# Performance work log

Hardware: AMD Instinct MI355X
Metric: run time of the kernel (lower is better)

Reference implementation:

```python
import jax, jax.numpy as jnp
import numpy as np

START_IDX = 1  # PAD_IDX = 0, END_IDX = 2 (unused in teacher-forcing path)
B, N, F = 16, 49, 1024
H, E, V = 1024, 1024, 15000
S, W = 5, 12


def setup_inputs() -> dict:
    key = jax.random.key(0)
    ks = jax.random.split(key, 16)
    def w(k, shape, s=0.02):
        return jax.random.normal(k, shape, dtype=jnp.float32) * s
    emb = w(ks[0], (V, E)).at[0].set(0.0)  # padding_idx = 0
    return dict(
        features=jax.random.normal(ks[1], (B, N, F), dtype=jnp.float32),
        reports=jax.random.randint(ks[2], (B, S, W), 0, V),
        attn_w1=w(ks[3], (F + H, H)), attn_b1=jnp.zeros((H,), jnp.float32),
        attn_w2=w(ks[4], (H, 1)), attn_b2=jnp.zeros((1,), jnp.float32),
        s_wih=w(ks[5], (4 * H, F)), s_whh=w(ks[6], (4 * H, H)),
        s_bih=jnp.zeros((4 * H,), jnp.float32), s_bhh=jnp.zeros((4 * H,), jnp.float32),
        stop_w=w(ks[7], (H, 1)), stop_b=jnp.zeros((1,), jnp.float32),
        emb=emb,
        w_wih=w(ks[8], (4 * H, E)), w_whh=w(ks[9], (4 * H, H)),
        w_bih=jnp.zeros((4 * H,), jnp.float32), w_bhh=jnp.zeros((4 * H,), jnp.float32),
        fc_w=w(ks[10], (H, V)), fc_b=jnp.zeros((V,), jnp.float32),
    )


def _lstm_cell(x, h, c, wih, whh, bih, bhh):
    # PyTorch LSTMCell: gates ordered i, f, g, o
    gates = x @ wih.T + h @ whh.T + (bih + bhh)
    i, f, g, o = jnp.split(gates, 4, axis=-1)
    c = jax.nn.sigmoid(f) * c + jax.nn.sigmoid(i) * jnp.tanh(g)
    h = jax.nn.sigmoid(o) * jnp.tanh(c)
    return h, c


def _attention(features, h, w1, b1, w2, b2):
    # features [B,N,F], h [B,H] -> additive 2-layer attention over N locations
    b, n, _ = features.shape
    hcat = jnp.broadcast_to(h[:, None, :], (b, n, h.shape[-1]))
    x = jnp.concatenate([features, hcat], axis=-1)           # [B,N,F+H]
    e = (jnp.tanh(x @ w1 + b1) @ w2 + b2)[..., 0]            # [B,N]
    scores = jax.nn.softmax(e, axis=-1)
    att = jnp.einsum('bn,bnf->bf', scores, features)          # [B,F]
    return att, scores


def _forward(features, reports, attn_w1, attn_b1, attn_w2, attn_b2,
             s_wih, s_whh, s_bih, s_bhh, stop_w, stop_b, emb,
             w_wih, w_whh, w_bih, w_bhh, fc_w, fc_b):
    bsz = features.shape[0]
    h0 = jnp.zeros((bsz, s_whh.shape[-1]), features.dtype)
    att0, _ = _attention(features, h0, attn_w1, attn_b1, attn_w2, attn_b2)
    start_emb = jnp.broadcast_to(emb[START_IDX][None, :], (bsz, emb.shape[-1]))

    def sentence_step(carry, reports_i):   # reports_i: [W, B] teacher-forcing tokens
        h, c, att = carry
        h, c = _lstm_cell(att, h, c, s_wih, s_whh, s_bih, s_bhh)
        czero = jnp.zeros_like(h)

        def word_step(wc, idx):
            hw, cw, inp = wc
            hw, cw = _lstm_cell(inp, hw, cw, w_wih, w_whh, w_bih, w_bhh)
            pred = hw @ fc_w + fc_b                           # [B,V]
            return (hw, cw, emb[idx]), pred

        # word LSTM initialized with h=topic, c=0; first input = <start> embedding
        _, preds = jax.lax.scan(word_step, (h, czero, start_emb), reports_i)  # [W,B,V]
        stop = jax.nn.sigmoid(h @ stop_w + stop_b)[:, 0]      # [B]
        att, scores = _attention(features, h, attn_w1, attn_b1, attn_w2, attn_b2)
        return (h, c, att), (preds, stop, scores)

    reports_sw = jnp.transpose(reports, (1, 2, 0))            # [S,W,B]
    _, (seq, stops, scores) = jax.lax.scan(sentence_step, (h0, h0, att0), reports_sw)
    seq_out = jnp.transpose(seq, (2, 0, 1, 3))                # [B,S,W,V]
    stops_out = jnp.transpose(stops, (1, 0))                  # [B,S]
    scores_out = jnp.transpose(scores, (1, 0, 2))             # [B,S,N]
    return seq_out, stops_out, scores_out


def reference(features, reports, attn_w1, attn_b1, attn_w2, attn_b2,
              s_wih, s_whh, s_bih, s_bhh, stop_w, stop_b, emb,
              w_wih, w_whh, w_bih, w_bhh, fc_w, fc_b):
    return _forward(features, reports, attn_w1, attn_b1, attn_w2, attn_b2,
                    s_wih, s_whh, s_bih, s_bhh, stop_w, stop_b, emb,
                    w_wih, w_whh, w_bih, w_bhh, fc_w, fc_b)
```

## Files before the change

kernel.cpp:

```cpp
#include <hip/hip_runtime.h>
#include <hip/hip_bf16.h>

#define B_  16
#define S_  5
#define W_  12
#define NL_ 49
#define H_  1024
#define V_  15000
#define SEQ_N   14400000
#define STOP_N  80
#define OUT_STOP (SEQ_N)
#define OUT_SCORE (SEQ_N + STOP_N)

typedef __attribute__((ext_vector_type(8))) short     short8;
typedef __attribute__((ext_vector_type(4))) float     f32x4;
typedef __attribute__((ext_vector_type(4))) unsigned int u32x4;
typedef __attribute__((ext_vector_type(4))) unsigned short us4;

#define OFF_FCWT   0ull
#define OFF_WWHHP  30720000ull
#define OFF_WWIHP  39108608ull
#define OFF_WSCATP 47497216ull
#define OFF_W1AT   64274432ull
#define OFF_W1BT   66371584ull
#define OFF_FBF    68468736ull
#define OFF_XIN    70074368ull
#define OFF_PF     72040448ull
#define OFF_XW     75251712ull
#define OFF_HBALL  90980352ull
#define OFF_HWBF0  92946432ull
#define OFF_HWBF1  93110272ull
#define OFF_ACAT1  93274112ull
#define OFF_H      93339648ull
#define OFF_EVAL   93405184ull
#define OFF_ACAT0  93408384ull
#define OFF_C      93473920ull
#define OFF_CW     93539456ull
#define OFF_HPROJ  93867136ull
#define WS_TOTAL   93932672ull
#define ZERO_BASE  OFF_ACAT0
#define ZERO_BYTES (524288ull)

__device__ __forceinline__ unsigned short f2bf(float x){
  unsigned u = __float_as_uint(x);
  u += 0x7fffu + ((u >> 16) & 1u);
  return (unsigned short)(u >> 16);
}
__device__ __forceinline__ float sigm(float x){ return 1.f/(1.f+expf(-x)); }

typedef __attribute__((address_space(3))) unsigned int  as3_u32;
typedef __attribute__((address_space(1))) const unsigned int as1_u32;

__device__ __forceinline__ void gl16(const void* g, void* l){
  __builtin_amdgcn_global_load_lds((as1_u32*)g, (as3_u32*)l, 16, 0, 0);
}

template<int ROWS,int CH,int NW>
__device__ __forceinline__ void stage_swz(const unsigned short* __restrict__ gbase, int grs,
                                          unsigned short* lds, int wid, int lane,
                                          int r0, int rmax){
  constexpr int RPI = 64/CH;
  constexpr int NISS = ROWS/RPI;
  const int r_in = lane / CH;
  const int cbp  = lane % CH;
  #pragma unroll
  for (int it = wid; it < NISS; it += NW){
    int rl = it*RPI + r_in;
    int gr = r0 + rl; gr = gr < rmax ? gr : rmax-1;
    int cb = cbp ^ (rl & 7);
    gl16(gbase + (size_t)gr*grs + cb*8, lds + it*RPI*CH*8);
  }
}

__device__ __forceinline__ void transp64(const float* __restrict__ src, int sld,
                                         int rb, int cb, int Cc,
                                         unsigned short* __restrict__ dst, int dld,
                                         float (*t)[65])
{
  const int tx = threadIdx.x & 15, ty = threadIdx.x >> 4;
  #pragma unroll
  for (int ii = 0; ii < 4; ii++){
    int r = ty + ii*16;
    int c = cb + tx*4;
    const float* s = src + (size_t)(rb + r)*sld + c;
    f32x4 v;
    if (c + 4 <= Cc) v = *(const f32x4*)s;
    else {
      v[0] = (c   < Cc) ? s[0] : 0.f;
      v[1] = (c+1 < Cc) ? s[1] : 0.f;
      v[2] = (c+2 < Cc) ? s[2] : 0.f;
      v[3] = (c+3 < Cc) ? s[3] : 0.f;
    }
    t[r][tx*4+0]=v[0]; t[r][tx*4+1]=v[1]; t[r][tx*4+2]=v[2]; t[r][tx*4+3]=v[3];
  }
  __syncthreads();
  #pragma unroll
  for (int ii = 0; ii < 4; ii++){
    int c = ty + ii*16;
    if (cb + c < Cc){
      int r4 = tx*4;
      us4 o; o[0]=f2bf(t[r4][c]); o[1]=f2bf(t[r4+1][c]); o[2]=f2bf(t[r4+2][c]); o[3]=f2bf(t[r4+3][c]);
      *(us4*)(dst + (size_t)(cb + c)*dld + rb + r4) = o;
    }
  }
}

#define U0 200704u
#define U1 (U0+1048576u)
#define U2 (U1+1048576u)
#define U3 (U2+1048576u)
#define U4 (U3+1048576u)
#define U5 (U4+245760u)
#define NCVT_BLK 1280
#define NTR_BLK  1068
#define NZ_BLK   16
#define NPREP    (NCVT_BLK + NTR_BLK + NZ_BLK)

__device__ __forceinline__ void cvt_gate_unit(const float* __restrict__ src,
                                              unsigned short* __restrict__ dst,
                                              unsigned e, int dld, int doff){
  int n = e >> 8, cc = (e & 255)*4;
  int gate = (n >> 4) & 3, j = ((n >> 6) << 4) | (n & 15);
  f32x4 v = *(const f32x4*)(src + ((size_t)(gate*1024 + j) << 10) + cc);
  us4 o; o[0]=f2bf(v[0]); o[1]=f2bf(v[1]); o[2]=f2bf(v[2]); o[3]=f2bf(v[3]);
  *(us4*)(dst + (size_t)n*dld + doff + cc) = o;
}

__global__ void k_prep(const float* __restrict__ features,
                       const float* __restrict__ w_whh, const float* __restrict__ w_wih,
                       const float* __restrict__ s_wih, const float* __restrict__ s_whh,
                       const float* __restrict__ emb, const int* __restrict__ reports,
                       const float* __restrict__ attn_w1, const float* __restrict__ fc_w,
                       unsigned short* __restrict__ FBF, unsigned short* __restrict__ WWHHP,
                       unsigned short* __restrict__ WWIHP, unsigned short* __restrict__ WSCATP,
                       unsigned short* __restrict__ XIN,
                       unsigned short* __restrict__ W1AT, unsigned short* __restrict__ W1BT,
                       unsigned short* __restrict__ FCWT, char* __restrict__ zbase)
{
  __shared__ float t[64][65];
  int bx = blockIdx.x;
  if (bx < NCVT_BLK){
    for (unsigned u = bx*256u + threadIdx.x; u < U5; u += NCVT_BLK*256u){
      if (u < U0){
        int idx = u*4;
        f32x4 v = *(const f32x4*)(features + idx);
        us4 o; o[0]=f2bf(v[0]); o[1]=f2bf(v[1]); o[2]=f2bf(v[2]); o[3]=f2bf(v[3]);
        *(us4*)(FBF + idx) = o;
      } else if (u < U1){
        cvt_gate_unit(w_whh, WWHHP, u - U0, 1024, 0);
      } else if (u < U2){
        cvt_gate_unit(w_wih, WWIHP, u - U1, 1024, 0);
      } else if (u < U3){
        cvt_gate_unit(s_wih, WSCATP, u - U2, 2048, 0);
      } else if (u < U4){
        cvt_gate_unit(s_whh, WSCATP, u - U3, 2048, 1024);
      } else {
        unsigned e = u - U4;
        int m = e >> 8, k = (e & 255)*4;
        int w = m / 80, r = m % 80, s = r >> 4, b = r & 15;
        int tok = (w == 0) ? 1 : reports[b*60 + s*12 + (w-1)];
        f32x4 v = *(const f32x4*)(emb + ((size_t)tok << 10) + k);
        us4 o; o[0]=f2bf(v[0]); o[1]=f2bf(v[1]); o[2]=f2bf(v[2]); o[3]=f2bf(v[3]);
        *(us4*)(XIN + (size_t)m*1024 + k) = o;
      }
    }
  } else if (bx < NCVT_BLK + NTR_BLK){
    int base = (bx - NCVT_BLK)*4;
    #pragma unroll
    for (int bt = 0; bt < 4; bt++){
      if (bt) __syncthreads();
      int tile = base + bt;
      if (tile < 512){
        int z = tile >> 8, rem = tile & 255;
        int rb = (rem & 15)*64, cb = (rem >> 4)*64;
        transp64(attn_w1 + (size_t)z*1024*1024, 1024, rb, cb, 1024, z ? W1BT : W1AT, 1024, t);
      } else {
        int ft = tile - 512;
        int rb = (ft & 15)*64, cb = (ft >> 4)*64;
        transp64(fc_w, V_, rb, cb, V_, FCWT, 1024, t);
      }
    }
  } else {
    int idx = bx - (NCVT_BLK + NTR_BLK);
    #pragma unroll
    for (int it = 0; it < 8; it++){
      size_t off = ((size_t)(idx + it*NZ_BLK))*4096 + threadIdx.x*16;
      *(u32x4*)(zbase + off) = (u32x4){0u,0u,0u,0u};
    }
  }
}

template<int BM,int BN,int BK,int WM,int WN,int EPI>
__global__ void k_gemm(const unsigned short* __restrict__ A, int lda,
                       const unsigned short* __restrict__ Bt, int ldb,
                       float* __restrict__ C, int ldc,
                       const float* __restrict__ bias,
                       int M, int N, int K)
{
  constexpr int NWV = WM*WN;
  constexpr int CH = BK/8;
  __shared__ __align__(16) unsigned short As[BM*BK];
  __shared__ __align__(16) unsigned short Bs[BN*BK];
  const int n0 = blockIdx.x * BN, m0 = blockIdx.y * BM;
  if (n0 >= N) return;
  const int tid  = threadIdx.x;
  const int lane = tid & 63;
  const int wave = tid >> 6;
  constexpr int WROWS = BM/WM, WCOLS = BN/WN;
  constexpr int FM = WROWS/16, FN = WCOLS/16;
  const int wm = wave / WN, wn = wave % WN;
  const int g = lane >> 4, fr = lane & 15;
  const int sx = fr & 7;

  f32x4 acc[FM][FN];
  #pragma unroll
  for (int a=0;a<FM;a++)
    #pragma unroll
    for (int b=0;b<FN;b++) acc[a][b] = (f32x4){0.f,0.f,0.f,0.f};

  for (int k0 = 0; k0 < K; k0 += BK) {
    if (k0) __syncthreads();
    stage_swz<BM,CH,NWV>(A + k0, lda, As, wave, lane, m0, M);
    stage_swz<BN,CH,NWV>(Bt + k0, ldb, Bs, wave, lane, n0, N);
    __syncthreads();
    #pragma unroll
    for (int kk = 0; kk < BK; kk += 32) {
      const int so = ((kk/8 + g) ^ sx) * 8;
      short8 af[FM], bt[FN];
      #pragma unroll
      for (int fm=0; fm<FM; fm++)
        af[fm] = *(const short8*)(As + (wm*WROWS + fm*16 + fr)*BK + so);
      #pragma unroll
      for (int fn=0; fn<FN; fn++)
        bt[fn] = *(const short8*)(Bs + (wn*WCOLS + fn*16 + fr)*BK + so);
      #pragma unroll
      for (int fm=0; fm<FM; fm++)
        #pragma unroll
        for (int fn=0; fn<FN; fn++)
          acc[fm][fn] = __builtin_amdgcn_mfma_f32_16x16x32_bf16(af[fm], bt[fn], acc[fm][fn], 0, 0, 0);
    }
  }

  #pragma unroll
  for (int fm=0; fm<FM; fm++)
    #pragma unroll
    for (int fn=0; fn<FN; fn++)
      #pragma unroll
      for (int j=0; j<4; j++){
        int m = m0 + wm*WROWS + fm*16 + g*4 + j;
        int n = n0 + wn*WCOLS + fn*16 + fr;
        if (m < M && n < N) {
          float v = acc[fm][fn][j];
          if (EPI == 1 || EPI == 2) v += bias[n];
          if (EPI == 2) {
            int b = m & 15, s = (m >> 4) % 5, w = m / 80;
            __builtin_nontemporal_store(v, &C[(size_t)((b*5 + s)*12 + w)*V_ + n]);
          } else if (EPI == 3) {
            __builtin_nontemporal_store(v, &C[(size_t)m*ldc + n]);
          } else {
            C[(size_t)m*ldc + n] = v;
          }
        }
      }
}

template<int BM,int BN,int BK,int WN,int SENT>
__global__ void k_gemm_cell(const unsigned short* __restrict__ A, int lda,
                            const unsigned short* __restrict__ Bt, int ldb,
                            const float* __restrict__ Xg, int ldx,
                            const float* __restrict__ bih, const float* __restrict__ bhh,
                            float* __restrict__ cst,
                            unsigned short* __restrict__ h1, int ldh1,
                            unsigned short* __restrict__ h2,
                            float* __restrict__ hf,
                            int M, int K)
{
  constexpr int CH = BK/8;
  __shared__ __align__(16) unsigned short As[BM*BK];
  __shared__ __align__(16) unsigned short Bs[BN*BK];
  const int tid  = threadIdx.x;
  const int lane = tid & 63;
  const int wn   = tid >> 6;
  const int n0 = blockIdx.x * BN, m0 = blockIdx.y * BM;
  const int g = lane >> 4, fr = lane & 15;
  const int sx = fr & 7;

  f32x4 acc[4];
  #pragma unroll
  for (int b=0;b<4;b++) acc[b] = (f32x4){0.f,0.f,0.f,0.f};

  for (int k0 = 0; k0 < K; k0 += BK) {
    if (k0) __syncthreads();
    stage_swz<BM,CH,WN>(A + k0, lda, As, wn, lane, m0, M);
    stage_swz<BN,CH,WN>(Bt + k0, ldb, Bs, wn, lane, n0, 4096);
    __syncthreads();
    #pragma unroll
    for (int kk = 0; kk < BK; kk += 32) {
      const int so = ((kk/8 + g) ^ sx) * 8;
      short8 af = *(const short8*)(As + fr*BK + so);
      #pragma unroll
      for (int fn=0; fn<4; fn++){
        short8 bt = *(const short8*)(Bs + (wn*64 + fn*16 + fr)*BK + so);
        acc[fn] = __builtin_amdgcn_mfma_f32_16x16x32_bf16(af, bt, acc[fn], 0, 0, 0);
      }
    }
  }

  const int nb = n0 + wn*64 + fr;
  const int j  = ((n0 + wn*64) >> 2) + fr;
  const float b0 = bih[j]        + bhh[j];
  const float b1 = bih[1024 + j] + bhh[1024 + j];
  const float b2 = bih[2048 + j] + bhh[2048 + j];
  const float b3 = bih[3072 + j] + bhh[3072 + j];
  #pragma unroll
  for (int jj=0; jj<4; jj++){
    int m = m0 + g*4 + jj;
    if (m < M){
      float gi = acc[0][jj] + b0;
      float gf = acc[1][jj] + b1;
      float gg = acc[2][jj] + b2;
      float go = acc[3][jj] + b3;
      if (!SENT){
        const float* xg = Xg + (size_t)m*ldx + nb;
        gi += xg[0]; gf += xg[16]; gg += xg[32]; go += xg[48];
      }
      float cn = sigm(gf)*cst[m*1024 + j] + sigm(gi)*tanhf(gg);
      float hn = sigm(go)*tanhf(cn);
      cst[m*1024 + j] = cn;
      unsigned short hb = f2bf(hn);
      h1[(size_t)m*ldh1 + j] = hb;
      h2[(size_t)m*1024 + j] = hb;
      if (SENT) hf[m*1024 + j] = hn;
    }
  }
}

__global__ void k_attn_e(const float* __restrict__ PF, const float* __restrict__ hproj,
                         const float* __restrict__ w2, float* __restrict__ evals)
{
  const int bn = blockIdx.x;
  const int b  = bn / NL_;
  const int tid = threadIdx.x;
  __shared__ float red[4];
  const float* pf = PF + ((size_t)bn << 10);
  const float* hp = hproj + (b << 10);
  int k = tid * 4;
  f32x4 a = *(const f32x4*)(pf + k);
  f32x4 hh = *(const f32x4*)(hp + k);
  f32x4 w = *(const f32x4*)(w2 + k);
  float p = tanhf(a[0]+hh[0])*w[0] + tanhf(a[1]+hh[1])*w[1]
          + tanhf(a[2]+hh[2])*w[2] + tanhf(a[3]+hh[3])*w[3];
  #pragma unroll
  for (int o = 32; o; o >>= 1) p += __shfl_down(p, o, 64);
  if ((tid & 63) == 0) red[tid >> 6] = p;
  __syncthreads();
  if (tid == 0) evals[bn] = red[0] + red[1] + red[2] + red[3];
}

template<int INIT>
__global__ void k_attn_fin(const float* __restrict__ evals, const float* __restrict__ features,
                           const float* __restrict__ h, const float* __restrict__ stop_w,
                           const float* __restrict__ stop_b,
                           unsigned short* __restrict__ Acat, float* __restrict__ outp, int s)
{
  const int b = blockIdx.x, tid = threadIdx.x;
  __shared__ float scs[64];
  __shared__ float red[4];
  if (tid < 64){
    float e = (tid < NL_) ? evals[b*NL_ + tid] : -1e30f;
    float mx = e;
    #pragma unroll
    for (int o = 32; o; o >>= 1) mx = fmaxf(mx, __shfl_xor(mx, o, 64));
    float ex = (tid < NL_) ? expf(e - mx) : 0.f;
    float dn = ex;
    #pragma unroll
    for (int o = 32; o; o >>= 1) dn += __shfl_xor(dn, o, 64);
    float sc = ex / dn;
    if (tid < NL_){
      scs[tid] = sc;
      if (!INIT) outp[OUT_SCORE + (b*5 + s)*NL_ + tid] = sc;
    }
  }
  __syncthreads();
  {
    int f0 = tid * 4;
    f32x4 a = (f32x4){0.f,0.f,0.f,0.f};
    const float* fb = features + (((size_t)b*NL_) << 10) + f0;
    #pragma unroll 7
    for (int n = 0; n < NL_; n++){
      f32x4 v = *(const f32x4*)(fb + ((size_t)n << 10));
      float sc = scs[n];
      a[0] += sc*v[0]; a[1] += sc*v[1]; a[2] += sc*v[2]; a[3] += sc*v[3];
    }
    us4 o4; o4[0]=f2bf(a[0]); o4[1]=f2bf(a[1]); o4[2]=f2bf(a[2]); o4[3]=f2bf(a[3]);
    *(us4*)(Acat + b*2048 + f0) = o4;
  }
  if (!INIT){
    int k = tid * 4;
    f32x4 hv = *(const f32x4*)(h + (b << 10) + k);
    f32x4 sw = *(const f32x4*)(stop_w + k);
    float p = hv[0]*sw[0] + hv[1]*sw[1] + hv[2]*sw[2] + hv[3]*sw[3];
    #pragma unroll
    for (int o = 32; o; o >>= 1) p += __shfl_down(p, o, 64);
    if ((tid & 63) == 0) red[tid >> 6] = p;
    __syncthreads();
    if (tid == 0) outp[OUT_STOP + b*5 + s] = sigm(red[0]+red[1]+red[2]+red[3] + stop_b[0]);
  }
}

extern "C" void kernel_launch(void* const* d_in, const int* in_sizes, int n_in,
                              void* d_out, int out_size, void* d_ws, size_t ws_size,
                              hipStream_t stream)
{
  const float* features = (const float*)d_in[0];
  const int*   reports  = (const int*)d_in[1];
  const float* attn_w1  = (const float*)d_in[2];
  const float* attn_b1  = (const float*)d_in[3];
  const float* attn_w2  = (const float*)d_in[4];
  const float* s_wih    = (const float*)d_in[6];
  const float* s_whh    = (const float*)d_in[7];
  const float* s_bih    = (const float*)d_in[8];
  const float* s_bhh    = (const float*)d_in[9];
  const float* stop_w   = (const float*)d_in[10];
  const float* stop_b   = (const float*)d_in[11];
  const float* emb      = (const float*)d_in[12];
  const float* w_wih    = (const float*)d_in[13];
  const float* w_whh    = (const float*)d_in[14];
  const float* w_bih    = (const float*)d_in[15];
  const float* w_bhh    = (const float*)d_in[16];
  const float* fc_w     = (const float*)d_in[17];
  const float* fc_b     = (const float*)d_in[18];
  float* out = (float*)d_out;
  char*  ws  = (char*)d_ws;
  if (ws_size < WS_TOTAL) return;

  unsigned short* FCWT   = (unsigned short*)(ws + OFF_FCWT);
  unsigned short* WWHHP  = (unsigned short*)(ws + OFF_WWHHP);
  unsigned short* WWIHP  = (unsigned short*)(ws + OFF_WWIHP);
  unsigned short* WSCATP = (unsigned short*)(ws + OFF_WSCATP);
  unsigned short* W1AT   = (unsigned short*)(ws + OFF_W1AT);
  unsigned short* W1BT   = (unsigned short*)(ws + OFF_W1BT);
  unsigned short* FBF    = (unsigned short*)(ws + OFF_FBF);
  unsigned short* XIN    = (unsigned short*)(ws + OFF_XIN);
  float*          PF     = (float*)(ws + OFF_PF);
  float*          XW     = (float*)(ws + OFF_XW);
  unsigned short* HBALL  = (unsigned short*)(ws + OFF_HBALL);
  unsigned short* HW0    = (unsigned short*)(ws + OFF_HWBF0);
  unsigned short* HW1    = (unsigned short*)(ws + OFF_HWBF1);
  unsigned short* ACAT0  = (unsigned short*)(ws + OFF_ACAT0);
  unsigned short* ACAT1  = (unsigned short*)(ws + OFF_ACAT1);
  float*          Hst    = (float*)(ws + OFF_H);
  float*          Cst    = (float*)(ws + OFF_C);
  float*          CW     = (float*)(ws + OFF_CW);
  float*          HPROJ  = (float*)(ws + OFF_HPROJ);
  float*          EVAL   = (float*)(ws + OFF_EVAL);

  k_prep<<<NPREP, 256, 0, stream>>>(features, w_whh, w_wih, s_wih, s_whh, emb, reports,
                                    attn_w1, fc_w,
                                    FBF, WWHHP, WWIHP, WSCATP, XIN, W1AT, W1BT, FCWT,
                                    ws + ZERO_BASE);

  k_gemm<64,64,128,2,2,1><<<dim3(16,13), 256, 0, stream>>>(FBF,1024, W1AT,1024, PF,1024, attn_b1, 784,1024,1024);
  k_gemm<64,128,128,2,2,3><<<dim3(32,15), 256, 0, stream>>>(XIN,1024, WWIHP,1024, XW,4096, nullptr, 960,4096,1024);

  k_attn_e<<<784, 256, 0, stream>>>(PF, HPROJ, attn_w2, EVAL);
  k_attn_fin<1><<<16, 256, 0, stream>>>(EVAL, features, Hst, stop_w, stop_b, ACAT0, out, 0);

  unsigned short* ACS[2] = {ACAT0, ACAT1};
  for (int s = 0; s < S_; s++){
    unsigned short* cur = ACS[s & 1];
    unsigned short* nxt = ACS[(s + 1) & 1];
    k_gemm_cell<16,128,128,2,1><<<dim3(32,1), 128, 0, stream>>>(
        cur, 2048, WSCATP, 2048, nullptr, 0, s_bih, s_bhh, Cst,
        nxt + 1024, 2048, HW0 + s*16*1024, Hst, 16, 2048);
    k_gemm<16,64,256,1,4,0><<<dim3(16,1), 256, 0, stream>>>(
        nxt + 1024, 2048, W1BT, 1024, HPROJ, 1024, nullptr, 16, 1024, 1024);
    k_attn_e<<<784, 256, 0, stream>>>(PF, HPROJ, attn_w2, EVAL);
    k_attn_fin<0><<<16, 256, 0, stream>>>(EVAL, features, Hst, stop_w, stop_b, nxt, out, s);
  }

  unsigned short* HW[2] = {HW0, HW1};
  for (int w = 0; w < W_; w++){
    k_gemm_cell<16,128,128,2,0><<<dim3(32,5), 128, 0, stream>>>(
        HW[w & 1], 1024, WWHHP, 1024, XW + (size_t)w*80*4096, 4096, w_bih, w_bhh, CW,
        HW[(w + 1) & 1], 1024, HBALL + (size_t)w*80*1024, nullptr, 80, 1024);
  }

  k_gemm<64,128,64,2,2,2><<<dim3(120,15), 256, 0, stream>>>(HBALL,1024, FCWT,1024, out,V_, fc_b, 960,15000,1024);
}
```

Measured before the change: 526.8 us.

## Double-buffer the final vocab projection GEMM and widen prep conversion per thread

```diff
diff --git a/kernel.cpp b/kernel.cpp
--- a/kernel.cpp
+++ b/kernel.cpp
@@ -55,6 +55,13 @@
   __builtin_amdgcn_global_load_lds((as1_u32*)g, (as3_u32*)l, 16, 0, 0);
 }
 
+template<int N> __device__ __forceinline__ void waitv(){
+  if constexpr (N==0)      asm volatile("s_waitcnt vmcnt(0)" ::: "memory");
+  else if constexpr (N==3) asm volatile("s_waitcnt vmcnt(3)" ::: "memory");
+  else if constexpr (N==6) asm volatile("s_waitcnt vmcnt(6)" ::: "memory");
+  else                     asm volatile("s_waitcnt vmcnt(0)" ::: "memory");
+}
+
 template<int ROWS,int CH,int NW>
 __device__ __forceinline__ void stage_swz(const unsigned short* __restrict__ gbase, int grs,
                                           unsigned short* lds, int wid, int lane,
@@ -105,13 +112,13 @@
   }
 }
 
-#define U0 200704u
-#define U1 (U0+1048576u)
-#define U2 (U1+1048576u)
-#define U3 (U2+1048576u)
-#define U4 (U3+1048576u)
-#define U5 (U4+245760u)
-#define NCVT_BLK 1280
+#define V0 200704u
+#define V1 1249280u
+#define V2 2297856u
+#define V3 3346432u
+#define V4 4395008u
+#define V5 4640768u
+#define NCVT_BLK 1133
 #define NTR_BLK  1068
 #define NZ_BLK   16
 #define NPREP    (NCVT_BLK + NTR_BLK + NZ_BLK)
@@ -140,28 +147,32 @@
   __shared__ float t[64][65];
   int bx = blockIdx.x;
   if (bx < NCVT_BLK){
-    for (unsigned u = bx*256u + threadIdx.x; u < U5; u += NCVT_BLK*256u){
-      if (u < U0){
-        int idx = u*4;
-        f32x4 v = *(const f32x4*)(features + idx);
-        us4 o; o[0]=f2bf(v[0]); o[1]=f2bf(v[1]); o[2]=f2bf(v[2]); o[3]=f2bf(v[3]);
-        *(us4*)(FBF + idx) = o;
-      } else if (u < U1){
-        cvt_gate_unit(w_whh, WWHHP, u - U0, 1024, 0);
-      } else if (u < U2){
-        cvt_gate_unit(w_wih, WWIHP, u - U1, 1024, 0);
-      } else if (u < U3){
-        cvt_gate_unit(s_wih, WSCATP, u - U2, 2048, 0);
-      } else if (u < U4){
-        cvt_gate_unit(s_whh, WSCATP, u - U3, 2048, 1024);
-      } else {
-        unsigned e = u - U4;
-        int m = e >> 8, k = (e & 255)*4;
-        int w = m / 80, r = m % 80, s = r >> 4, b = r & 15;
-        int tok = (w == 0) ? 1 : reports[b*60 + s*12 + (w-1)];
-        f32x4 v = *(const f32x4*)(emb + ((size_t)tok << 10) + k);
-        us4 o; o[0]=f2bf(v[0]); o[1]=f2bf(v[1]); o[2]=f2bf(v[2]); o[3]=f2bf(v[3]);
-        *(us4*)(XIN + (size_t)m*1024 + k) = o;
+    for (unsigned base = bx*1024u + threadIdx.x*4u; base < V5; base += NCVT_BLK*1024u){
+      #pragma unroll
+      for (int q = 0; q < 4; q++){
+        unsigned u = base + q;
+        if (u < V0){
+          int idx = u*4;
+          f32x4 v = *(const f32x4*)(features + idx);
+          us4 o; o[0]=f2bf(v[0]); o[1]=f2bf(v[1]); o[2]=f2bf(v[2]); o[3]=f2bf(v[3]);
+          *(us4*)(FBF + idx) = o;
+        } else if (u < V1){
+          cvt_gate_unit(w_whh, WWHHP, u - V0, 1024, 0);
+        } else if (u < V2){
+          cvt_gate_unit(w_wih, WWIHP, u - V1, 1024, 0);
+        } else if (u < V3){
+          cvt_gate_unit(s_wih, WSCATP, u - V2, 2048, 0);
+        } else if (u < V4){
+          cvt_gate_unit(s_whh, WSCATP, u - V3, 2048, 1024);
+        } else {
+          unsigned e = u - V4;
+          int m = e >> 8, k = (e & 255)*4;
+          int w = m / 80, r = m % 80, s = r >> 4, b = r & 15;
+          int tok = (w == 0) ? 1 : reports[b*60 + s*12 + (w-1)];
+          f32x4 v = *(const f32x4*)(emb + ((size_t)tok << 10) + k);
+          us4 o; o[0]=f2bf(v[0]); o[1]=f2bf(v[1]); o[2]=f2bf(v[2]); o[3]=f2bf(v[3]);
+          *(us4*)(XIN + (size_t)m*1024 + k) = o;
+        }
       }
     }
   } else if (bx < NCVT_BLK + NTR_BLK){
@@ -251,15 +262,91 @@
         int n = n0 + wn*WCOLS + fn*16 + fr;
         if (m < M && n < N) {
           float v = acc[fm][fn][j];
-          if (EPI == 1 || EPI == 2) v += bias[n];
-          if (EPI == 2) {
-            int b = m & 15, s = (m >> 4) % 5, w = m / 80;
-            __builtin_nontemporal_store(v, &C[(size_t)((b*5 + s)*12 + w)*V_ + n]);
-          } else if (EPI == 3) {
-            __builtin_nontemporal_store(v, &C[(size_t)m*ldc + n]);
-          } else {
-            C[(size_t)m*ldc + n] = v;
-          }
+          if (EPI == 1) v += bias[n];
+          if (EPI == 3) __builtin_nontemporal_store(v, &C[(size_t)m*ldc + n]);
+          else          C[(size_t)m*ldc + n] = v;
+        }
+      }
+}
+
+template<int BM,int BN,int BK,int WM,int WN>
+__global__ void k_fc(const unsigned short* __restrict__ A, int lda,
+                     const unsigned short* __restrict__ Bt, int ldb,
+                     float* __restrict__ C,
+                     const float* __restrict__ bias,
+                     int M, int N, int K)
+{
+  constexpr int NWV = WM*WN;
+  constexpr int CH = BK/8;
+  constexpr int LPW = (BM*CH/64)/NWV + (BN*CH/64)/NWV;
+  static_assert(LPW == 6, "vmcnt literal must match");
+  __shared__ __align__(16) unsigned short As[2][BM*BK];
+  __shared__ __align__(16) unsigned short Bs[2][BN*BK];
+  const int n0 = blockIdx.x * BN, m0 = blockIdx.y * BM;
+  const int tid  = threadIdx.x;
+  const int lane = tid & 63;
+  const int wave = tid >> 6;
+  constexpr int WROWS = BM/WM, WCOLS = BN/WN;
+  constexpr int FM = WROWS/16, FN = WCOLS/16;
+  const int wm = wave / WN, wn = wave % WN;
+  const int g = lane >> 4, fr = lane & 15;
+  const int sx = fr & 7;
+
+  f32x4 acc[FM][FN];
+  #pragma unroll
+  for (int a=0;a<FM;a++)
+    #pragma unroll
+    for (int b=0;b<FN;b++) acc[a][b] = (f32x4){0.f,0.f,0.f,0.f};
+
+  stage_swz<BM,CH,NWV>(A, lda, As[0], wave, lane, m0, M);
+  stage_swz<BN,CH,NWV>(Bt, ldb, Bs[0], wave, lane, n0, N);
+
+  for (int k0 = 0; k0 < K; k0 += BK) {
+    const int t = (k0/BK) & 1;
+    if (k0 + BK < K) {
+      stage_swz<BM,CH,NWV>(A + k0 + BK, lda, As[t^1], wave, lane, m0, M);
+      stage_swz<BN,CH,NWV>(Bt + k0 + BK, ldb, Bs[t^1], wave, lane, n0, N);
+      waitv<6>();
+    } else {
+      waitv<0>();
+    }
+    __builtin_amdgcn_sched_barrier(0);
+    __builtin_amdgcn_s_barrier();
+    __builtin_amdgcn_sched_barrier(0);
+    __builtin_amdgcn_s_setprio(1);
+    #pragma unroll
+    for (int kk = 0; kk < BK; kk += 32) {
+      const int so = ((kk/8 + g) ^ sx) * 8;
+      short8 af[FM], bt[FN];
+      #pragma unroll
+      for (int fm=0; fm<FM; fm++)
+        af[fm] = *(const short8*)(As[t] + (wm*WROWS + fm*16 + fr)*BK + so);
+      #pragma unroll
+      for (int fn=0; fn<FN; fn++)
+        bt[fn] = *(const short8*)(Bs[t] + (wn*WCOLS + fn*16 + fr)*BK + so);
+      #pragma unroll
+      for (int fm=0; fm<FM; fm++)
+        #pragma unroll
+        for (int fn=0; fn<FN; fn++)
+          acc[fm][fn] = __builtin_amdgcn_mfma_f32_16x16x32_bf16(af[fm], bt[fn], acc[fm][fn], 0, 0, 0);
+    }
+    __builtin_amdgcn_s_setprio(0);
+    __builtin_amdgcn_sched_barrier(0);
+    __builtin_amdgcn_s_barrier();
+  }
+
+  #pragma unroll
+  for (int fm=0; fm<FM; fm++)
+    #pragma unroll
+    for (int fn=0; fn<FN; fn++)
+      #pragma unroll
+      for (int j=0; j<4; j++){
+        int m = m0 + wm*WROWS + fm*16 + g*4 + j;
+        int n = n0 + wn*WCOLS + fn*16 + fr;
+        if (m < M && n < N) {
+          float v = acc[fm][fn][j] + bias[n];
+          int b = m & 15, s = (m >> 4) % 5, w = m / 80;
+          __builtin_nontemporal_store(v, &C[(size_t)((b*5 + s)*12 + w)*V_ + n]);
         }
       }
 }
@@ -486,5 +573,5 @@
         HW[(w + 1) & 1], 1024, HBALL + (size_t)w*80*1024, nullptr, 80, 1024);
   }
 
-  k_gemm<64,128,64,2,2,2><<<dim3(120,15), 256, 0, stream>>>(HBALL,1024, FCWT,1024, out,V_, fc_b, 960,15000,1024);
-}
+  k_fc<64,128,64,2,2><<<dim3(120,15), 256, 0, stream>>>(HBALL,1024, FCWT,1024, out, fc_b, 960,15000,1024);
+}
```

New measurement: 564.5 us. 1.07x slower.

## Double-buffer LDS tiles in LSTM cell GEMM with async prefetch

Applied to the files above, without the earlier changes.

```diff
diff --git a/kernel.cpp b/kernel.cpp
--- a/kernel.cpp
+++ b/kernel.cpp
@@ -53,6 +53,12 @@
 
 __device__ __forceinline__ void gl16(const void* g, void* l){
   __builtin_amdgcn_global_load_lds((as1_u32*)g, (as3_u32*)l, 16, 0, 0);
+}
+
+template<int N> __device__ __forceinline__ void waitv(){
+  if constexpr (N==0)       asm volatile("s_waitcnt vmcnt(0)"  ::: "memory");
+  else if constexpr (N==18) asm volatile("s_waitcnt vmcnt(18)" ::: "memory");
+  else                      asm volatile("s_waitcnt vmcnt(0)"  ::: "memory");
 }
 
 template<int ROWS,int CH,int NW>
@@ -276,8 +282,10 @@
                             int M, int K)
 {
   constexpr int CH = BK/8;
-  __shared__ __align__(16) unsigned short As[BM*BK];
-  __shared__ __align__(16) unsigned short Bs[BN*BK];
+  constexpr int LPW = (BM*CH/64)/WN + (BN*CH/64)/WN;
+  static_assert(LPW == 18, "vmcnt literal must match");
+  __shared__ __align__(16) unsigned short As[2][BM*BK];
+  __shared__ __align__(16) unsigned short Bs[2][BN*BK];
   const int tid  = threadIdx.x;
   const int lane = tid & 63;
   const int wn   = tid >> 6;
@@ -289,21 +297,33 @@
   #pragma unroll
   for (int b=0;b<4;b++) acc[b] = (f32x4){0.f,0.f,0.f,0.f};
 
+  stage_swz<BM,CH,WN>(A, lda, As[0], wn, lane, m0, M);
+  stage_swz<BN,CH,WN>(Bt, ldb, Bs[0], wn, lane, n0, 4096);
+
   for (int k0 = 0; k0 < K; k0 += BK) {
-    if (k0) __syncthreads();
-    stage_swz<BM,CH,WN>(A + k0, lda, As, wn, lane, m0, M);
-    stage_swz<BN,CH,WN>(Bt + k0, ldb, Bs, wn, lane, n0, 4096);
-    __syncthreads();
+    const int t = (k0/BK) & 1;
+    if (k0 + BK < K) {
+      stage_swz<BM,CH,WN>(A + k0 + BK, lda, As[t^1], wn, lane, m0, M);
+      stage_swz<BN,CH,WN>(Bt + k0 + BK, ldb, Bs[t^1], wn, lane, n0, 4096);
+      waitv<18>();
+    } else {
+      waitv<0>();
+    }
+    __builtin_amdgcn_sched_barrier(0);
+    __builtin_amdgcn_s_barrier();
+    __builtin_amdgcn_sched_barrier(0);
     #pragma unroll
     for (int kk = 0; kk < BK; kk += 32) {
       const int so = ((kk/8 + g) ^ sx) * 8;
-      short8 af = *(const short8*)(As + fr*BK + so);
+      short8 af = *(const short8*)(As[t] + fr*BK + so);
       #pragma unroll
       for (int fn=0; fn<4; fn++){
-        short8 bt = *(const short8*)(Bs + (wn*64 + fn*16 + fr)*BK + so);
+        short8 bt = *(const short8*)(Bs[t] + (wn*64 + fn*16 + fr)*BK + so);
         acc[fn] = __builtin_amdgcn_mfma_f32_16x16x32_bf16(af, bt, acc[fn], 0, 0, 0);
       }
     }
+    __builtin_amdgcn_sched_barrier(0);
+    __builtin_amdgcn_s_barrier();
   }
 
   const int nb = n0 + wn*64 + fr;
```

Result: no change. 533.8 us (+1.3%).

## Replace final vocab projection GEMM with 256x256 double-buffered tiled kernel

Applied to the files above, without the earlier changes.

```diff
diff --git a/kernel.cpp b/kernel.cpp
--- a/kernel.cpp
+++ b/kernel.cpp
@@ -53,6 +53,12 @@
 
 __device__ __forceinline__ void gl16(const void* g, void* l){
   __builtin_amdgcn_global_load_lds((as1_u32*)g, (as3_u32*)l, 16, 0, 0);
+}
+
+template<int N> __device__ __forceinline__ void waitv(){
+  if constexpr (N==0)      asm volatile("s_waitcnt vmcnt(0)" ::: "memory");
+  else if constexpr (N==8) asm volatile("s_waitcnt vmcnt(8)" ::: "memory");
+  else                     asm volatile("s_waitcnt vmcnt(0)" ::: "memory");
 }
 
 template<int ROWS,int CH,int NW>
@@ -251,15 +257,90 @@
         int n = n0 + wn*WCOLS + fn*16 + fr;
         if (m < M && n < N) {
           float v = acc[fm][fn][j];
-          if (EPI == 1 || EPI == 2) v += bias[n];
-          if (EPI == 2) {
-            int b = m & 15, s = (m >> 4) % 5, w = m / 80;
-            __builtin_nontemporal_store(v, &C[(size_t)((b*5 + s)*12 + w)*V_ + n]);
-          } else if (EPI == 3) {
-            __builtin_nontemporal_store(v, &C[(size_t)m*ldc + n]);
-          } else {
-            C[(size_t)m*ldc + n] = v;
-          }
+          if (EPI == 1) v += bias[n];
+          if (EPI == 3) __builtin_nontemporal_store(v, &C[(size_t)m*ldc + n]);
+          else          C[(size_t)m*ldc + n] = v;
+        }
+      }
+}
+
+__global__ void __launch_bounds__(512,2) k_fc256(
+    const unsigned short* __restrict__ A, int lda,
+    const unsigned short* __restrict__ Bt, int ldb,
+    float* __restrict__ C, const float* __restrict__ bias,
+    int M, int N)
+{
+  constexpr int NK = 16;
+  __shared__ __align__(16) unsigned short As[2*256*64];
+  __shared__ __align__(16) unsigned short Bs[2*256*64];
+  const int bid = blockIdx.x, x = bid & 7, lid = bid >> 3;
+  if (x >= 4 && lid >= 29) return;
+  const int t = (x < 4) ? x*30 + lid : 120 + (x-4)*29 + lid;
+  const int n0 = (t >> 2) * 256, m0 = (t & 3) * 256;
+
+  const int tid  = threadIdx.x;
+  const int lane = tid & 63;
+  const int wave = tid >> 6;
+  const int wr = wave >> 2, wc = wave & 3;
+  const int g = lane >> 4, fr = lane & 15;
+  const int sx = fr & 7;
+
+  f32x4 acc[8][4];
+  #pragma unroll
+  for (int a=0;a<8;a++)
+    #pragma unroll
+    for (int b=0;b<4;b++) acc[a][b] = (f32x4){0.f,0.f,0.f,0.f};
+
+  stage_swz<256,8,8>(A,        lda, As,          wave, lane, m0, M);
+  stage_swz<256,8,8>(Bt,       ldb, Bs,          wave, lane, n0, N);
+  stage_swz<256,8,8>(A  + 64,  lda, As + 256*64, wave, lane, m0, M);
+  stage_swz<256,8,8>(Bt + 64,  ldb, Bs + 256*64, wave, lane, n0, N);
+
+  for (int k = 0; k < NK; k++){
+    unsigned short* As_c = As + (k & 1)*(256*64);
+    unsigned short* Bs_c = Bs + (k & 1)*(256*64);
+    if (k == NK-1) waitv<0>(); else waitv<8>();
+    __builtin_amdgcn_sched_barrier(0);
+    __builtin_amdgcn_s_barrier();
+    __builtin_amdgcn_sched_barrier(0);
+    __builtin_amdgcn_s_setprio(1);
+    #pragma unroll
+    for (int kk = 0; kk < 64; kk += 32){
+      const int so = ((kk/8 + g) ^ sx) * 8;
+      short8 af[8], bt[4];
+      #pragma unroll
+      for (int fn=0; fn<4; fn++)
+        bt[fn] = *(const short8*)(Bs_c + (wc*64 + fn*16 + fr)*64 + so);
+      #pragma unroll
+      for (int fm=0; fm<8; fm++)
+        af[fm] = *(const short8*)(As_c + (wr*128 + fm*16 + fr)*64 + so);
+      #pragma unroll
+      for (int fm=0; fm<8; fm++)
+        #pragma unroll
+        for (int fn=0; fn<4; fn++)
+          acc[fm][fn] = __builtin_amdgcn_mfma_f32_16x16x32_bf16(af[fm], bt[fn], acc[fm][fn], 0, 0, 0);
+    }
+    __builtin_amdgcn_s_setprio(0);
+    __builtin_amdgcn_sched_barrier(0);
+    __builtin_amdgcn_s_barrier();
+    if (k + 2 < NK){
+      stage_swz<256,8,8>(A  + (k+2)*64, lda, As_c, wave, lane, m0, M);
+      stage_swz<256,8,8>(Bt + (k+2)*64, ldb, Bs_c, wave, lane, n0, N);
+    }
+  }
+
+  #pragma unroll
+  for (int fm=0; fm<8; fm++)
+    #pragma unroll
+    for (int fn=0; fn<4; fn++)
+      #pragma unroll
+      for (int j=0; j<4; j++){
+        int m = m0 + wr*128 + fm*16 + g*4 + j;
+        int n = n0 + wc*64 + fn*16 + fr;
+        if (m < M && n < N){
+          float v = acc[fm][fn][j] + bias[n];
+          int b = m & 15, s = (m >> 4) % 5, w = m / 80;
+          __builtin_nontemporal_store(v, &C[(size_t)((b*5 + s)*12 + w)*V_ + n]);
         }
       }
 }
@@ -486,5 +567,5 @@
         HW[(w + 1) & 1], 1024, HBALL + (size_t)w*80*1024, nullptr, 80, 1024);
   }
 
-  k_gemm<64,128,64,2,2,2><<<dim3(120,15), 256, 0, stream>>>(HBALL,1024, FCWT,1024, out,V_, fc_b, 960,15000,1024);
-}
+  k_fc256<<<240, 512, 0, stream>>>(HBALL,1024, FCWT,1024, out, fc_b, 960, 15000);
+}
```

After: 538.6 us. 1.02x slower.
